# Kernel tuning notes

Hardware: AMD Instinct MI355X
Metric: run time of the kernel (lower is better)

## Reference

```python
import jax, jax.numpy as jnp
import numpy as np
import math

MODEL_DIM = 2048
NUM_Q_HEADS = 32
NUM_KV_HEADS = 8
HEAD_DIM = 64
ROPE_BASE = 10000.0
RMS_EPS = 1e-6


def setup_inputs() -> dict:
    key = jax.random.key(0)
    k1, k2, k3 = jax.random.split(key, 3)
    B, S = 2, 2048
    std = MODEL_DIM ** -0.5
    qkv_out = (NUM_Q_HEADS + 2 * NUM_KV_HEADS) * HEAD_DIM  # 3072
    return {
        "x": jax.random.normal(k1, (B, S, MODEL_DIM), dtype=jnp.float32),
        "w_qkv": jax.random.normal(k2, (qkv_out, MODEL_DIM), dtype=jnp.float32) * std,
        "w_out": jax.random.normal(k3, (MODEL_DIM, NUM_Q_HEADS * HEAD_DIM), dtype=jnp.float32) * std,
        "q_gamma": jnp.ones((HEAD_DIM,), dtype=jnp.float32),
        "k_gamma": jnp.ones((HEAD_DIM,), dtype=jnp.float32),
    }


def _rms_norm(x, gamma):
    # weight * sqrt(d) * F.normalize(x, dim=-1, eps): x / max(||x||_2, eps)
    norm = jnp.sqrt(jnp.sum(x * x, axis=-1, keepdims=True))
    scale = HEAD_DIM ** 0.5
    return (gamma * scale) * x / jnp.maximum(norm, RMS_EPS)


def _rope(x):
    # x: [B, H, S, hd]; rotate-half style RoPE, offset=0
    S = x.shape[2]
    half = HEAD_DIM // 2
    pos = jnp.arange(S, dtype=x.dtype)
    freqs = jnp.exp(-jnp.arange(half, dtype=x.dtype) * (math.log(ROPE_BASE) / half))
    theta = pos[:, None] * freqs[None, :]  # [S, half]
    sin, cos = jnp.sin(theta), jnp.cos(theta)
    x1, x2 = x[..., :half], x[..., half:]
    return jnp.concatenate([x1 * cos - x2 * sin, x1 * sin + x2 * cos], axis=-1)


def reference(x, w_qkv, w_out, q_gamma, k_gamma):
    B, S, D = x.shape
    groups = NUM_Q_HEADS // NUM_KV_HEADS
    qkv = jnp.einsum("bsd,ed->bse", x, w_qkv)  # [B,S,3072]
    qkv = qkv.reshape(B, S, NUM_Q_HEADS + 2 * NUM_KV_HEADS, HEAD_DIM).transpose(0, 2, 1, 3)
    q = qkv[:, :NUM_Q_HEADS]                                 # [B,Hq,S,hd]
    k = qkv[:, NUM_Q_HEADS:NUM_Q_HEADS + NUM_KV_HEADS]       # [B,Hk,S,hd]
    v = qkv[:, NUM_Q_HEADS + NUM_KV_HEADS:]                  # [B,Hk,S,hd]
    q = _rope(_rms_norm(q, q_gamma))
    k = _rope(_rms_norm(k, k_gamma))
    # GQA: repeat_interleave over head dim
    k = jnp.repeat(k, groups, axis=1)  # [B,Hq,S,hd]
    v = jnp.repeat(v, groups, axis=1)
    scale = 1.0 / (HEAD_DIM ** 0.5)
    scores = jnp.einsum("bhqd,bhkd->bhqk", q, k) * scale
    causal = jnp.tril(jnp.ones((S, S), dtype=bool))
    scores = jnp.where(causal, scores, jnp.finfo(scores.dtype).min)
    attn = jax.nn.softmax(scores, axis=-1)
    out = jnp.einsum("bhqk,bhkd->bhqd", attn, v)             # [B,Hq,S,hd]
    out = out.transpose(0, 2, 1, 3).reshape(B, S, NUM_Q_HEADS * HEAD_DIM)
    return jnp.einsum("bse,de->bsd", out, w_out)
```

## Files before the change

kernel.cpp:

```cpp
#include <hip/hip_runtime.h>
#include <hip/hip_bf16.h>
#include <stdint.h>

#define S_LEN  2048
#define BATCH  2
#define DMODEL 2048
#define EQKV   3072
#define HQ     32
#define HKV    8
#define HD     64
#define MROWS  (BATCH * S_LEN)

typedef unsigned short u16;
typedef __attribute__((ext_vector_type(8))) short bf16x8;
typedef __attribute__((ext_vector_type(4))) short bf16x4;
typedef __attribute__((ext_vector_type(4))) float f32x4;

__device__ __forceinline__ u16 f2bf(float f) {
  uint32_t x = __builtin_bit_cast(uint32_t, f);
  uint32_t r = x + 0x7fffu + ((x >> 16) & 1u);
  return (u16)(r >> 16);
}
__device__ __forceinline__ short f2bf_s(float f) {
  return __builtin_bit_cast(short, __float2bfloat16(f));
}
__device__ __forceinline__ float b2f(u16 u) {
  uint32_t x = ((uint32_t)u) << 16;
  return __builtin_bit_cast(float, x);
}
__device__ __forceinline__ float bflo(uint32_t u) {
  uint32_t x = u << 16; return __builtin_bit_cast(float, x);
}
__device__ __forceinline__ float bfhi(uint32_t u) {
  uint32_t x = u & 0xffff0000u; return __builtin_bit_cast(float, x);
}
__device__ __forceinline__ float fexp2(float x) {
#if __has_builtin(__builtin_amdgcn_exp2f)
  return __builtin_amdgcn_exp2f(x);
#else
  return exp2f(x);
#endif
}

__device__ __forceinline__ void gld16(const void* g, void* l) {
  __builtin_amdgcn_global_load_lds(
      (const __attribute__((address_space(1))) void*)g,
      (__attribute__((address_space(3))) void*)l, 16, 0, 0);
}

#define N8_X  ((size_t)MROWS * DMODEL / 8)
#define N8_WQ ((size_t)EQKV * DMODEL / 8)
#define N8_WO ((size_t)DMODEL * DMODEL / 8)
__global__ void cast3(const float* __restrict__ xa, const float* __restrict__ xb,
                      const float* __restrict__ xc,
                      u16* __restrict__ oa, u16* __restrict__ ob, u16* __restrict__ oc) {
  const int ntot = (int)(N8_X + N8_WQ + N8_WO);
  int stride = gridDim.x * blockDim.x;
  for (int i = blockIdx.x * blockDim.x + threadIdx.x; i < ntot; i += stride) {
    const float* in;
    u16* out;
    int j = i;
    if (j < (int)N8_X)                { in = xa; out = oa; }
    else if (j < (int)(N8_X + N8_WQ)) { in = xb; out = ob; j -= (int)N8_X; }
    else                              { in = xc; out = oc; j -= (int)(N8_X + N8_WQ); }
    const float4* p = (const float4*)(in + (size_t)j * 8);
    float4 a = p[0], b = p[1];
    uint32_t u0 = (uint32_t)f2bf(a.x) | ((uint32_t)f2bf(a.y) << 16);
    uint32_t u1 = (uint32_t)f2bf(a.z) | ((uint32_t)f2bf(a.w) << 16);
    uint32_t u2 = (uint32_t)f2bf(b.x) | ((uint32_t)f2bf(b.y) << 16);
    uint32_t u3 = (uint32_t)f2bf(b.z) | ((uint32_t)f2bf(b.w) << 16);
    *(uint4*)(out + (size_t)j * 8) = make_uint4(u0, u1, u2, u3);
  }
}

template<int OUT_BF16>
__global__ __launch_bounds__(256) void gemm_bt(const u16* __restrict__ A,
                                               const u16* __restrict__ Bm,
                                               void* __restrict__ Cv,
                                               int M, int N, int K, int nbx) {
  __shared__ u16 lA[128 * 64];
  __shared__ u16 lB[128 * 64];
  const int tid  = threadIdx.x;
  const int wave = tid >> 6;
  const int lane = tid & 63;

  const int nwg = gridDim.x;
  const int wg  = blockIdx.x;
  const int swz = (wg & 7) * (nwg >> 3) + (wg >> 3);
  const int brow = (swz % nbx) * 128;
  const int bcol = (swz / nbx) * 128;

  const int wr = (wave >> 1) * 64;
  const int wc = (wave & 1) * 64;
  const int fr = lane & 15;
  const int fq = lane >> 4;

  const int srow8 = lane >> 3;
  const int scol  = ((lane & 7) ^ srow8) * 8;

  f32x4 acc[4][4];
#pragma unroll
  for (int i = 0; i < 4; ++i)
#pragma unroll
    for (int j = 0; j < 4; ++j) acc[i][j] = (f32x4){0.f, 0.f, 0.f, 0.f};

  for (int k0 = 0; k0 < K; k0 += 64) {
    __syncthreads();
#pragma unroll
    for (int j = 0; j < 4; ++j) {
      int c = wave * 4 + j;
      int r = c * 8 + srow8;
      gld16(A  + (size_t)(brow + r) * K + k0 + scol, (char*)lA + c * 1024);
      gld16(Bm + (size_t)(bcol + r) * K + k0 + scol, (char*)lB + c * 1024);
    }
    __syncthreads();

    bf16x8 af[2][4], bfr[2][4];
#pragma unroll
    for (int kc = 0; kc < 2; ++kc) {
#pragma unroll
      for (int i = 0; i < 4; ++i) {
        int row = wr + i * 16 + fr;
        af[kc][i] = *(const bf16x8*)&lA[row * 64 + (((kc * 4 + fq) ^ (row & 7)) << 3)];
      }
#pragma unroll
      for (int j = 0; j < 4; ++j) {
        int row = wc + j * 16 + fr;
        bfr[kc][j] = *(const bf16x8*)&lB[row * 64 + (((kc * 4 + fq) ^ (row & 7)) << 3)];
      }
    }
#pragma unroll
    for (int kc = 0; kc < 2; ++kc)
#pragma unroll
      for (int i = 0; i < 4; ++i)
#pragma unroll
        for (int j = 0; j < 4; ++j)
          acc[i][j] = __builtin_amdgcn_mfma_f32_16x16x32_bf16(af[kc][i], bfr[kc][j], acc[i][j], 0, 0, 0);
  }

#pragma unroll
  for (int i = 0; i < 4; ++i)
#pragma unroll
    for (int j = 0; j < 4; ++j)
#pragma unroll
      for (int v = 0; v < 4; ++v) {
        int row = brow + wr + i * 16 + fq * 4 + v;
        int col = bcol + wc + j * 16 + fr;
        float val = acc[i][j][v];
        if (OUT_BF16) ((u16*)Cv)[(size_t)row * N + col] = f2bf(val);
        else          ((float*)Cv)[(size_t)row * N + col] = val;
      }
}

__global__ __launch_bounds__(256) void rmsrope(const u16* __restrict__ qkv,
                                               u16* __restrict__ Qb,
                                               u16* __restrict__ Kb,
                                               const float* __restrict__ qg,
                                               const float* __restrict__ kg) {
  int wid  = blockIdx.x * 4 + (threadIdx.x >> 6);
  int lane = threadIdx.x & 63;
  int head = wid % 40;
  int bs   = wid / 40;
  int s    = bs & (S_LEN - 1);
  int b    = bs >> 11;

  float v = b2f(qkv[(size_t)bs * EQKV + head * HD + lane]);
  float ss = v * v;
#pragma unroll
  for (int msk = 32; msk >= 1; msk >>= 1) ss += __shfl_xor(ss, msk);
  float norm = sqrtf(ss);
  float g = (head < 32) ? qg[lane] : kg[lane];
  float xv = v * (8.0f * g / fmaxf(norm, 1e-6f));
  float prt = __shfl_xor(xv, 32);
  int i = lane & 31;
  float freq  = expf(-(float)i * 0.28782313662425572f);
  float theta = (float)s * freq;
  float sn = sinf(theta), cs = cosf(theta);
  float res = (lane < 32) ? (xv * cs - prt * sn) : (prt * sn + xv * cs);
  u16 r = f2bf(res);
  if (head < 32) Qb[(((size_t)(b * HQ  + head     )) * S_LEN + s) * HD + lane] = r;
  else           Kb[(((size_t)(b * HKV + head - 32)) * S_LEN + s) * HD + lane] = r;
}

__global__ __launch_bounds__(256) void vtrans(const u16* __restrict__ qkv,
                                              u16* __restrict__ VTb) {
  __shared__ u16 T[64][68];
  const int bid   = blockIdx.x;
  const int stile = bid & 31;
  const int plane = bid >> 5;
  const int b = plane >> 3, kh = plane & 7;
  const int s0 = stile * 64;
  const int t = threadIdx.x;
  const int r = t >> 2, u0 = t & 3;

  const u16* src = qkv + ((size_t)(b * S_LEN + s0 + r)) * EQKV + (HQ + HKV + kh) * HD;
  *(uint4*)&T[r][u0 * 8]      = *(const uint4*)(src + u0 * 8);
  *(uint4*)&T[r][u0 * 8 + 32] = *(const uint4*)(src + u0 * 8 + 32);
  __syncthreads();

  const int d = t >> 2;
  u16* dst = VTb + ((size_t)plane * HD + d) * S_LEN + s0;
#pragma unroll
  for (int half = 0; half < 2; ++half) {
    int ub = u0 + half * 4;
    u16 tmp[8];
#pragma unroll
    for (int j = 0; j < 8; ++j) tmp[j] = T[ub * 8 + j][d];
    *(uint4*)(dst + ub * 8) = *(const uint4*)tmp;
  }
}

__global__ __launch_bounds__(128) void attn_mfma(const u16* __restrict__ Qb,
                                                 const u16* __restrict__ Kb,
                                                 const u16* __restrict__ VTb,
                                                 u16* __restrict__ Ob) {
  __shared__ u16 Ks[64 * 64];
  __shared__ u16 Vt[64 * 64];
  const int tid  = threadIdx.x;
  const int wv   = tid >> 6;
  const int lane = tid & 63;
  const int fr   = lane & 15;
  const int fq   = lane >> 4;
  const int bh   = blockIdx.x;
  const int b    = bh >> 5, h = bh & 31, kh = h >> 2;
  const size_t kvbase = ((size_t)(b * HKV + kh)) * S_LEN * HD;

  const int tile   = 31 - (int)blockIdx.y;
  const int wqmin  = tile * 64 + wv * 32;
  const int kv_end = tile * 64 + 64;

  const int srow  = lane >> 3;
  const int sunit = (lane & 7) ^ srow;
  const u16* kp0 = Kb  + kvbase + (size_t)(wv * 32 + srow) * HD    + sunit * 8;
  const u16* vp0 = VTb + kvbase + (size_t)(wv * 32 + srow) * S_LEN + sunit * 8;

  const float QSCALE = 0.18033688011112042f;
  bf16x8 aq[2][2];
#pragma unroll
  for (int qf = 0; qf < 2; ++qf)
#pragma unroll
    for (int kc = 0; kc < 2; ++kc) {
      const u16* qp = Qb + ((size_t)bh * S_LEN + (wqmin + qf * 16 + fr)) * HD + kc * 32 + fq * 8;
      uint4 u = *(const uint4*)qp;
      uint32_t w[4] = {u.x, u.y, u.z, u.w};
      bf16x8 r;
#pragma unroll
      for (int i = 0; i < 4; ++i) {
        r[2 * i]     = f2bf_s(bflo(w[i]) * QSCALE);
        r[2 * i + 1] = f2bf_s(bfhi(w[i]) * QSCALE);
      }
      aq[qf][kc] = r;
    }

  f32x4 o[2][4];
#pragma unroll
  for (int qf = 0; qf < 2; ++qf)
#pragma unroll
    for (int df = 0; df < 4; ++df) o[qf][df] = (f32x4){0.f, 0.f, 0.f, 0.f};
  float l_run[2] = {0.f, 0.f};

  for (int k0 = 0; k0 < kv_end; k0 += 64) {
    __syncthreads();
#pragma unroll
    for (int i = 0; i < 4; ++i)
      gld16(kp0 + (size_t)(k0 + i * 8) * HD, (char*)Ks + (wv * 4 + i) * 1024);
#pragma unroll
    for (int i = 0; i < 4; ++i)
      gld16(vp0 + k0 + (size_t)(i * 8) * S_LEN, (char*)Vt + (wv * 4 + i) * 1024);
    __syncthreads();

    f32x4 st[2][4];
#pragma unroll
    for (int qf = 0; qf < 2; ++qf)
#pragma unroll
      for (int kf = 0; kf < 4; ++kf) st[qf][kf] = (f32x4){0.f, 0.f, 0.f, 0.f};
    __builtin_amdgcn_s_setprio(1);
#pragma unroll
    for (int kf = 0; kf < 4; ++kf) {
      int row = kf * 16 + fr;
#pragma unroll
      for (int kc = 0; kc < 2; ++kc) {
        bf16x8 ak = *(const bf16x8*)((char*)Ks + row * 128 +
                                     ((kc * 64 + fq * 16) ^ ((row & 7) << 4)));
#pragma unroll
        for (int qf = 0; qf < 2; ++qf)
          st[qf][kf] = __builtin_amdgcn_mfma_f32_16x16x32_bf16(ak, aq[qf][kc], st[qf][kf], 0, 0, 0);
      }
    }
    __builtin_amdgcn_s_setprio(0);

    const bool need_mask = (k0 + 63 > wqmin);
    bf16x4 pb[2][4];
#pragma unroll
    for (int qf = 0; qf < 2; ++qf) {
      const int qrow = wqmin + qf * 16 + fr;
      if (need_mask) {
#pragma unroll
        for (int kf = 0; kf < 4; ++kf)
#pragma unroll
          for (int v = 0; v < 4; ++v) {
            int kvg = k0 + kf * 16 + fq * 4 + v;
            st[qf][kf][v] = (kvg > qrow) ? -1e30f : st[qf][kf][v];
          }
      }
      float acc_l = 0.f;
#pragma unroll
      for (int kf = 0; kf < 4; ++kf) {
        bf16x4 pp;
#pragma unroll
        for (int v = 0; v < 4; ++v) {
          float e = fexp2(st[qf][kf][v] - 12.0f);
          acc_l += e;
          pp[v] = f2bf_s(e);
        }
        pb[qf][kf] = pp;
      }
      l_run[qf] += acc_l;
    }

    __builtin_amdgcn_s_setprio(1);
#pragma unroll
    for (int df = 0; df < 4; ++df) {
      int row = df * 16 + fr;
#pragma unroll
      for (int kf = 0; kf < 4; ++kf) {
        bf16x4 av = *(const bf16x4*)((char*)Vt + row * 128 +
                                     ((kf * 32 + fq * 8) ^ ((row & 7) << 4)));
#pragma unroll
        for (int qf = 0; qf < 2; ++qf)
          o[qf][df] = __builtin_amdgcn_mfma_f32_16x16x16bf16_1k(av, pb[qf][kf], o[qf][df], 0, 0, 0);
      }
    }
    __builtin_amdgcn_s_setprio(0);
  }

#pragma unroll
  for (int qf = 0; qf < 2; ++qf) {
    float l = l_run[qf];
    l += __shfl_xor(l, 16);
    l += __shfl_xor(l, 32);
    float inv = 1.0f / l;
    int grow = b * S_LEN + wqmin + qf * 16 + fr;
#pragma unroll
    for (int df = 0; df < 4; ++df) {
      u16* op = Ob + (size_t)grow * DMODEL + h * HD + df * 16 + fq * 4;
      uint32_t w0 = (uint32_t)f2bf(o[qf][df][0] * inv) | ((uint32_t)f2bf(o[qf][df][1] * inv) << 16);
      uint32_t w1 = (uint32_t)f2bf(o[qf][df][2] * inv) | ((uint32_t)f2bf(o[qf][df][3] * inv) << 16);
      *(uint2*)op = make_uint2(w0, w1);
    }
  }
}

extern "C" void kernel_launch(void* const* d_in, const int* in_sizes, int n_in,
                              void* d_out, int out_size, void* d_ws, size_t ws_size,
                              hipStream_t stream) {
  const float* x    = (const float*)d_in[0];
  const float* wqkv = (const float*)d_in[1];
  const float* wout = (const float*)d_in[2];
  const float* qg   = (const float*)d_in[3];
  const float* kg   = (const float*)d_in[4];
  float* out = (float*)d_out;
  char* ws = (char*)d_ws;

  const size_t MB = 1024 * 1024;
  u16* xb    = (u16*)(ws + 0 * MB);
  u16* wqkvb = (u16*)(ws + 16 * MB);
  u16* qkvb  = (u16*)(ws + 28 * MB);
  u16* Qb    = (u16*)(ws + 52 * MB);
  u16* Kb    = (u16*)(ws + 68 * MB);
  u16* VTb   = (u16*)(ws + 72 * MB);
  u16* Ob    = xb;
  u16* woutb = (u16*)(ws + 76 * MB);

  cast3<<<2048, 256, 0, stream>>>(x, wqkv, wout, xb, wqkvb, woutb);
  gemm_bt<1><<<(MROWS / 128) * (EQKV / 128), 256, 0, stream>>>(xb, wqkvb, qkvb, MROWS, EQKV, DMODEL, MROWS / 128);
  rmsrope<<<(MROWS * 40) / 4, 256, 0, stream>>>(qkvb, Qb, Kb, qg, kg);
  vtrans<<<BATCH * HKV * 32, 256, 0, stream>>>(qkvb, VTb);
  attn_mfma<<<dim3(BATCH * HQ, 32), 128, 0, stream>>>(Qb, Kb, VTb, Ob);
  gemm_bt<0><<<(MROWS / 128) * (DMODEL / 128), 256, 0, stream>>>(Ob, woutb, out, MROWS, DMODEL, DMODEL, MROWS / 128);
}
```

Baseline: 224.2 us.

## Use 8-wave GEMM tiles and compute softmax row sums via MFMA

```diff
diff --git a/kernel.cpp b/kernel.cpp
--- a/kernel.cpp
+++ b/kernel.cpp
@@ -74,7 +74,7 @@
 }
 
 template<int OUT_BF16>
-__global__ __launch_bounds__(256) void gemm_bt(const u16* __restrict__ A,
+__global__ __launch_bounds__(512) void gemm_bt(const u16* __restrict__ A,
                                                const u16* __restrict__ Bm,
                                                void* __restrict__ Cv,
                                                int M, int N, int K, int nbx) {
@@ -90,32 +90,32 @@
   const int brow = (swz % nbx) * 128;
   const int bcol = (swz / nbx) * 128;
 
-  const int wr = (wave >> 1) * 64;
-  const int wc = (wave & 1) * 64;
+  const int wr = (wave >> 2) * 64;
+  const int wc = (wave & 3) * 32;
   const int fr = lane & 15;
   const int fq = lane >> 4;
 
   const int srow8 = lane >> 3;
   const int scol  = ((lane & 7) ^ srow8) * 8;
 
-  f32x4 acc[4][4];
+  f32x4 acc[4][2];
 #pragma unroll
   for (int i = 0; i < 4; ++i)
 #pragma unroll
-    for (int j = 0; j < 4; ++j) acc[i][j] = (f32x4){0.f, 0.f, 0.f, 0.f};
+    for (int j = 0; j < 2; ++j) acc[i][j] = (f32x4){0.f, 0.f, 0.f, 0.f};
 
   for (int k0 = 0; k0 < K; k0 += 64) {
     __syncthreads();
 #pragma unroll
-    for (int j = 0; j < 4; ++j) {
-      int c = wave * 4 + j;
+    for (int j = 0; j < 2; ++j) {
+      int c = wave * 2 + j;
       int r = c * 8 + srow8;
       gld16(A  + (size_t)(brow + r) * K + k0 + scol, (char*)lA + c * 1024);
       gld16(Bm + (size_t)(bcol + r) * K + k0 + scol, (char*)lB + c * 1024);
     }
     __syncthreads();
 
-    bf16x8 af[2][4], bfr[2][4];
+    bf16x8 af[2][4], bfr[2][2];
 #pragma unroll
     for (int kc = 0; kc < 2; ++kc) {
 #pragma unroll
@@ -124,7 +124,7 @@
         af[kc][i] = *(const bf16x8*)&lA[row * 64 + (((kc * 4 + fq) ^ (row & 7)) << 3)];
       }
 #pragma unroll
-      for (int j = 0; j < 4; ++j) {
+      for (int j = 0; j < 2; ++j) {
         int row = wc + j * 16 + fr;
         bfr[kc][j] = *(const bf16x8*)&lB[row * 64 + (((kc * 4 + fq) ^ (row & 7)) << 3)];
       }
@@ -134,14 +134,14 @@
 #pragma unroll
       for (int i = 0; i < 4; ++i)
 #pragma unroll
-        for (int j = 0; j < 4; ++j)
+        for (int j = 0; j < 2; ++j)
           acc[i][j] = __builtin_amdgcn_mfma_f32_16x16x32_bf16(af[kc][i], bfr[kc][j], acc[i][j], 0, 0, 0);
   }
 
 #pragma unroll
   for (int i = 0; i < 4; ++i)
 #pragma unroll
-    for (int j = 0; j < 4; ++j)
+    for (int j = 0; j < 2; ++j)
 #pragma unroll
       for (int v = 0; v < 4; ++v) {
         int row = brow + wr + i * 16 + fq * 4 + v;
@@ -252,12 +252,17 @@
       aq[qf][kc] = r;
     }
 
+  const f32x4 Z4 = (f32x4){0.f, 0.f, 0.f, 0.f};
+  bf16x4 ones;
+#pragma unroll
+  for (int v = 0; v < 4; ++v) ones[v] = (short)0x3F80;
+
   f32x4 o[2][4];
 #pragma unroll
   for (int qf = 0; qf < 2; ++qf)
 #pragma unroll
-    for (int df = 0; df < 4; ++df) o[qf][df] = (f32x4){0.f, 0.f, 0.f, 0.f};
-  float l_run[2] = {0.f, 0.f};
+    for (int df = 0; df < 4; ++df) o[qf][df] = Z4;
+  f32x4 lacc[2] = {Z4, Z4};
 
   for (int k0 = 0; k0 < kv_end; k0 += 64) {
     __syncthreads();
@@ -270,21 +275,18 @@
     __syncthreads();
 
     f32x4 st[2][4];
-#pragma unroll
-    for (int qf = 0; qf < 2; ++qf)
-#pragma unroll
-      for (int kf = 0; kf < 4; ++kf) st[qf][kf] = (f32x4){0.f, 0.f, 0.f, 0.f};
     __builtin_amdgcn_s_setprio(1);
 #pragma unroll
     for (int kf = 0; kf < 4; ++kf) {
       int row = kf * 16 + fr;
-#pragma unroll
-      for (int kc = 0; kc < 2; ++kc) {
-        bf16x8 ak = *(const bf16x8*)((char*)Ks + row * 128 +
-                                     ((kc * 64 + fq * 16) ^ ((row & 7) << 4)));
-#pragma unroll
-        for (int qf = 0; qf < 2; ++qf)
-          st[qf][kf] = __builtin_amdgcn_mfma_f32_16x16x32_bf16(ak, aq[qf][kc], st[qf][kf], 0, 0, 0);
+      bf16x8 ak0 = *(const bf16x8*)((char*)Ks + row * 128 +
+                                    ((fq * 16) ^ ((row & 7) << 4)));
+      bf16x8 ak1 = *(const bf16x8*)((char*)Ks + row * 128 +
+                                    ((64 + fq * 16) ^ ((row & 7) << 4)));
+#pragma unroll
+      for (int qf = 0; qf < 2; ++qf) {
+        f32x4 t = __builtin_amdgcn_mfma_f32_16x16x32_bf16(ak0, aq[qf][0], Z4, 0, 0, 0);
+        st[qf][kf] = __builtin_amdgcn_mfma_f32_16x16x32_bf16(ak1, aq[qf][1], t, 0, 0, 0);
       }
     }
     __builtin_amdgcn_s_setprio(0);
@@ -303,19 +305,13 @@
             st[qf][kf][v] = (kvg > qrow) ? -1e30f : st[qf][kf][v];
           }
       }
-      float acc_l = 0.f;
 #pragma unroll
       for (int kf = 0; kf < 4; ++kf) {
         bf16x4 pp;
 #pragma unroll
-        for (int v = 0; v < 4; ++v) {
-          float e = fexp2(st[qf][kf][v] - 12.0f);
-          acc_l += e;
-          pp[v] = f2bf_s(e);
-        }
+        for (int v = 0; v < 4; ++v) pp[v] = f2bf_s(fexp2(st[qf][kf][v]));
         pb[qf][kf] = pp;
       }
-      l_run[qf] += acc_l;
     }
 
     __builtin_amdgcn_s_setprio(1);
@@ -331,15 +327,17 @@
           o[qf][df] = __builtin_amdgcn_mfma_f32_16x16x16bf16_1k(av, pb[qf][kf], o[qf][df], 0, 0, 0);
       }
     }
+#pragma unroll
+    for (int kf = 0; kf < 4; ++kf)
+#pragma unroll
+      for (int qf = 0; qf < 2; ++qf)
+        lacc[qf] = __builtin_amdgcn_mfma_f32_16x16x16bf16_1k(ones, pb[qf][kf], lacc[qf], 0, 0, 0);
     __builtin_amdgcn_s_setprio(0);
   }
 
 #pragma unroll
   for (int qf = 0; qf < 2; ++qf) {
-    float l = l_run[qf];
-    l += __shfl_xor(l, 16);
-    l += __shfl_xor(l, 32);
-    float inv = 1.0f / l;
+    float inv = 1.0f / lacc[qf][0];
     int grow = b * S_LEN + wqmin + qf * 16 + fr;
 #pragma unroll
     for (int df = 0; df < 4; ++df) {
@@ -373,9 +371,9 @@
   u16* woutb = (u16*)(ws + 76 * MB);
 
   cast3<<<2048, 256, 0, stream>>>(x, wqkv, wout, xb, wqkvb, woutb);
-  gemm_bt<1><<<(MROWS / 128) * (EQKV / 128), 256, 0, stream>>>(xb, wqkvb, qkvb, MROWS, EQKV, DMODEL, MROWS / 128);
+  gemm_bt<1><<<(MROWS / 128) * (EQKV / 128), 512, 0, stream>>>(xb, wqkvb, qkvb, MROWS, EQKV, DMODEL, MROWS / 128);
   rmsrope<<<(MROWS * 40) / 4, 256, 0, stream>>>(qkvb, Qb, Kb, qg, kg);
   vtrans<<<BATCH * HKV * 32, 256, 0, stream>>>(qkvb, VTb);
   attn_mfma<<<dim3(BATCH * HQ, 32), 128, 0, stream>>>(Qb, Kb, VTb, Ob);
-  gemm_bt<0><<<(MROWS / 128) * (DMODEL / 128), 256, 0, stream>>>(Ob, woutb, out, MROWS, DMODEL, DMODEL, MROWS / 128);
-}
+  gemm_bt<0><<<(MROWS / 128) * (DMODEL / 128), 512, 0, stream>>>(Ob, woutb, out, MROWS, DMODEL, DMODEL, MROWS / 128);
+}
```

Measured after the change: 211.0 us. -5.9%, faster.
